# Kernel optimization log

Measured on AMD Instinct MI355X. Metric: run time of the kernel, lower is better.

Reference implementation:

```python
import jax, jax.numpy as jnp
import numpy as np


def pairwise_euclidean_distance(x, y):
    # x: [N, D], y: [K, D] -> [N, K] squared Euclidean distances
    cross = -2.0 * (x @ y.T)
    x_term = jnp.sum(x * x, axis=1, keepdims=True)      # [N, 1]
    y_term = jnp.sum(y * y, axis=1, keepdims=True).T    # [1, K]
    return cross + x_term + y_term


def quantize(z, centroids):
    # z: [B, T, D], centroids: [K, D]
    B, T, D = z.shape
    flat = z.reshape(-1, D)                              # [N, D]
    distances = pairwise_euclidean_distance(flat, centroids)
    alignment = jnp.argmin(distances, axis=1)            # [N]
    q = centroids[alignment]                             # gather [N, D]
    # straight-through estimator: grad flows to z, not centroids
    q = flat + jax.lax.stop_gradient(q - flat)
    return q.reshape(B, T, D)


def setup_inputs() -> dict:
    key = jax.random.key(0)
    ks = jax.random.split(key, 5)
    B, T, F, D, K = 16, 2048, 80, 512, 2048
    return {
        "x": jax.random.normal(ks[0], (B, T, F), dtype=jnp.float32),
        "W_enc": jax.random.normal(ks[1], (F, D), dtype=jnp.float32) * (1.0 / np.sqrt(F)),
        "b_enc": jnp.zeros((D,), dtype=jnp.float32),
        "centroids": jax.random.normal(ks[2], (K, D), dtype=jnp.float32),
        "W_dec": jax.random.normal(ks[3], (D, F), dtype=jnp.float32) * (1.0 / np.sqrt(D)),
        "b_dec": jnp.zeros((F,), dtype=jnp.float32),
    }


def reference(x, W_enc, b_enc, centroids, W_dec, b_dec):
    z = x @ W_enc + b_enc            # encoder: [B, T, D]
    zq = quantize(z, centroids)      # VQ: distance + argmin + gather
    out = zq @ W_dec + b_dec         # decoder: [B, T, F]
    return out
```

## Files before the change

kernel.cpp:

```cpp
#include <hip/hip_runtime.h>
#include <hip/hip_bf16.h>

#define N_TOK  32768
#define F_IN   80
#define D_DIM  512
#define K_CENT 2048
#define F_OUT  80
#define TM     16
#define KP     96
#define M2     0.5f
#define QSLOTS 24
#define QREC   200
#define TREC   800
#define JTOT   160

typedef __attribute__((ext_vector_type(8)))  short bf16x8;
typedef __attribute__((ext_vector_type(4)))  float fx4;
typedef __attribute__((ext_vector_type(16))) float fx16;

#define AS3 __attribute__((address_space(3)))
#define AS1 __attribute__((address_space(1)))

__device__ inline unsigned short f2bf(float f) {
    unsigned u = __float_as_uint(f);
    return (unsigned short)((u + 0x7FFFu + ((u >> 16) & 1u)) >> 16);
}
__device__ inline float bf2f(unsigned short h) {
    return __uint_as_float((unsigned)h << 16);
}

__device__ inline void gll16(const unsigned short* g, unsigned short* l) {
    __builtin_amdgcn_global_load_lds((const AS1 unsigned*)g, (AS3 unsigned*)l, 16, 0, 0);
}

__device__ inline unsigned fkey(float f) {
    unsigned b = __float_as_uint(f);
    return b ^ ((b >> 31) ? 0xFFFFFFFFu : 0x80000000u);
}
__device__ inline float keyf(unsigned k) {
    unsigned b = k ^ ((k & 0x80000000u) ? 0x80000000u : 0xFFFFFFFFu);
    return __uint_as_float(b);
}

__device__ inline size_t frag32_addr(int row, int k) {
    int sub = (row >> 5) * 2 + ((k >> 4) & 1);
    int L = (row & 31) + ((k >> 3) & 1) * 32;
    return (size_t)sub * 512 + L * 8 + (k & 7);
}

__global__ __launch_bounds__(256) void k_prep1(
    const float* __restrict__ x, const float* __restrict__ Wenc,
    const float* __restrict__ Wdec, const float* __restrict__ cent,
    const float* __restrict__ benc,
    unsigned short* __restrict__ xbt, float* __restrict__ Bcat,
    float* __restrict__ cnorm, unsigned short* __restrict__ Gbt) {
    const int bid = blockIdx.x, tid = threadIdx.x;
    if (bid < 1536) {
        int o = bid * 256 + tid;
        int m = o / 12;
        int ko = (o - m * 12) * 8;
        unsigned short u[8];
        if (ko < F_IN) {
            const float* src = x + (size_t)m * F_IN + ko;
            float4 v0 = *(const float4*)src;
            float4 v1 = *(const float4*)(src + 4);
            u[0]=f2bf(v0.x); u[1]=f2bf(v0.y); u[2]=f2bf(v0.z); u[3]=f2bf(v0.w);
            u[4]=f2bf(v1.x); u[5]=f2bf(v1.y); u[6]=f2bf(v1.z); u[7]=f2bf(v1.w);
        } else if (ko == 80) {
            u[0] = 0x3F80; u[1] = 0x3F80;
#pragma unroll
            for (int j = 2; j < 8; ++j) u[j] = 0;
        } else {
#pragma unroll
            for (int j = 0; j < 8; ++j) u[j] = 0;
        }
        int mt = m >> 7, kt = ko >> 5, row = m & 127, kl = ko & 31;
        uint4 p;
        p.x = (unsigned)u[0] | ((unsigned)u[1] << 16);
        p.y = (unsigned)u[2] | ((unsigned)u[3] << 16);
        p.z = (unsigned)u[4] | ((unsigned)u[5] << 16);
        p.w = (unsigned)u[6] | ((unsigned)u[7] << 16);
        *(uint4*)&xbt[(size_t)(mt * 3 + kt) * 4096 + frag32_addr(row, kl)] = p;
    } else if (bid < 1856) {
        int e = (bid - 1536) * 256 + tid;
        int d = e / JTOT, j = e - d * JTOT;
        float v = (j < F_OUT) ? Wdec[(size_t)d * F_OUT + j]
                              : Wenc[(size_t)(j - F_OUT) * D_DIM + d];
        Bcat[e] = v;
    } else {
        int wave = tid >> 6, lane = tid & 63;
        int k = (bid - 1856) * 4 + wave;
        const float* row = cent + (size_t)k * D_DIM;
        float s = 0.f, t = 0.f;
#pragma unroll
        for (int j = 0; j < 8; ++j) {
            float c = row[lane + 64 * j];
            float b = benc[lane + 64 * j];
            s += c * c; t += b * c;
        }
#pragma unroll
        for (int off = 32; off; off >>= 1) { s += __shfl_down(s, off); t += __shfl_down(t, off); }
        const int nt = k >> 7, cl = k & 127;
        const size_t tb = (size_t)(nt * 3 + 2) * 4096;
        if (lane < 14)
            Gbt[tb + frag32_addr(cl, 18 + lane)] = 0;
        if (lane == 0) {
            cnorm[k] = s;
            float v = -0.5f * (s - 2.0f * t);
            unsigned short h = f2bf(v);
            unsigned short l = f2bf(v - bf2f(h));
            Gbt[tb + frag32_addr(cl, 16)] = h;
            Gbt[tb + frag32_addr(cl, 17)] = l;
        }
    }
}

__global__ __launch_bounds__(384) void k_cgemm2(
    const float* __restrict__ cent, const float* __restrict__ Bcat,
    const float* __restrict__ bdec, unsigned short* __restrict__ Gbt,
    float* __restrict__ dec) {
    __shared__ float pacc[192][4];
    const int tid = threadIdx.x;
    const int j = tid % 192;
    const int dh = tid / 192;
    const int k0 = blockIdx.x * 4;
    float a0 = 0.f, a1 = 0.f, a2 = 0.f, a3 = 0.f;
    if (j < JTOT) {
        const float* c0 = cent + (size_t)k0 * D_DIM + dh * 256;
        const float* bp = Bcat + (size_t)dh * 256 * JTOT + j;
#pragma unroll 4
        for (int d = 0; d < 256; ++d) {
            float b  = bp[d * JTOT];
            a0 += c0[d] * b;
            a1 += c0[D_DIM + d] * b;
            a2 += c0[2 * D_DIM + d] * b;
            a3 += c0[3 * D_DIM + d] * b;
        }
        if (dh == 1) { pacc[j][0] = a0; pacc[j][1] = a1; pacc[j][2] = a2; pacc[j][3] = a3; }
    }
    __syncthreads();
    if (dh == 0 && j < JTOT) {
        a0 += pacc[j][0]; a1 += pacc[j][1]; a2 += pacc[j][2]; a3 += pacc[j][3];
        float a[4] = { a0, a1, a2, a3 };
        if (j < F_OUT) {
            float bd = bdec[j];
#pragma unroll
            for (int c = 0; c < 4; ++c)
                dec[(size_t)(k0 + c) * F_OUT + j] = a[c] + bd;
        } else {
            int f = j - F_OUT;
#pragma unroll
            for (int c = 0; c < 4; ++c) {
                int k = k0 + c;
                Gbt[(size_t)((k >> 7) * 3 + (f >> 5)) * 4096 + frag32_addr(k & 127, f & 31)]
                    = f2bf(a[c]);
            }
        }
    }
}

__global__ __launch_bounds__(512) void k_dist3(
    const unsigned short* __restrict__ xbt, const unsigned short* __restrict__ Gbt,
    char* __restrict__ lists) {
    __shared__ unsigned short Bs[2][12288];
    __shared__ int cnt[128];
    __shared__ unsigned mxk[128];

    const int tid = threadIdx.x;
    const int bid = blockIdx.x;
    const int mt = bid >> 2, nq = bid & 3;
    const int lane = tid & 63;
    const int wave = tid >> 6;
    const int tg = wave >> 1;
    const int ch = wave & 1;
    const int col = lane & 31;
    const int hi = lane >> 5;

    if (tid < 128) { cnt[tid] = 0; mxk[tid] = 0u; }

    bf16x8 bfr[6];
    const unsigned short* Ab = xbt + (size_t)mt * 12288;
#pragma unroll
    for (int kc = 0; kc < 6; ++kc)
        bfr[kc] = *(const bf16x8*)&Ab[(kc >> 1) * 4096 + (tg * 2 + (kc & 1)) * 512 + lane * 8];

    const int woff = (tid & ~63) * 8;
    const unsigned short* Gq = Gbt + (size_t)nq * 4 * 12288;
#pragma unroll
    for (int q = 0; q < 3; ++q)
        gll16(Gq + q * 4096 + tid * 8, &Bs[0][0] + q * 4096 + woff);

    float rmax = -3.4e38f;
    int cur = 0;
    for (int t4 = 0; t4 < 4; ++t4) {
        __syncthreads();
        if (t4 + 1 < 4) {
#pragma unroll
            for (int q = 0; q < 3; ++q)
                gll16(Gq + (size_t)(t4 + 1) * 12288 + q * 4096 + tid * 8,
                      &Bs[cur ^ 1][0] + q * 4096 + woff);
        }
        const unsigned short* B = &Bs[cur][0];
        fx16 acc[2];
#pragma unroll
        for (int u = 0; u < 2; ++u)
#pragma unroll
            for (int r = 0; r < 16; ++r) acc[u][r] = 0.f;
#pragma unroll
        for (int kc = 0; kc < 6; ++kc) {
#pragma unroll
            for (int u = 0; u < 2; ++u) {
                bf16x8 a = *(const bf16x8*)&B[(kc >> 1) * 4096
                             + ((ch * 2 + u) * 2 + (kc & 1)) * 512 + lane * 8];
                acc[u] = __builtin_amdgcn_mfma_f32_32x32x16_bf16(a, bfr[kc], acc[u], 0, 0, 0);
            }
        }
        float m = acc[0][0];
#pragma unroll
        for (int r = 1; r < 16; ++r) m = fmaxf(m, acc[0][r]);
#pragma unroll
        for (int r = 0; r < 16; ++r) m = fmaxf(m, acc[1][r]);
        m = fmaxf(m, __shfl_xor(m, 32));
        rmax = fmaxf(rmax, m);
        const float th = rmax - M2;
        const int tk = tg * 32 + col;
        char* qrec = lists + (size_t)(mt * 128 + tk) * TREC + nq * QREC;
#pragma unroll
        for (int u = 0; u < 2; ++u)
#pragma unroll
            for (int r = 0; r < 16; ++r) {
                float v = acc[u][r];
                if (v >= th) {
                    int slot = atomicAdd(&cnt[tk], 1);
                    if (slot < QSLOTS) {
                        uint2 e;
                        e.x = __float_as_uint(v);
                        e.y = (unsigned)((nq * 4 + t4) * 128 + (ch * 2 + u) * 32
                                         + (r & 3) + 8 * (r >> 2) + 4 * hi);
                        *(uint2*)(qrec + 8 + slot * 8) = e;
                    }
                }
            }
        cur ^= 1;
    }
    if (lane < 32) atomicMax(&mxk[tg * 32 + lane], fkey(rmax));
    __syncthreads();
    if (tid < 128) {
        uint2 h;
        h.x = (unsigned)cnt[tid];
        h.y = __float_as_uint(keyf(mxk[tid]));
        *(uint2*)(lists + (size_t)(mt * 128 + tid) * TREC + nq * QREC) = h;
    }
}

__global__ __launch_bounds__(256) void k_merge4(
    const char* __restrict__ lists, const float* __restrict__ cnorm,
    const float* __restrict__ cent, const float* __restrict__ x,
    const float* __restrict__ Wenc, const float* __restrict__ benc,
    const float* __restrict__ dec, float* __restrict__ out) {
    const int lane = threadIdx.x & 63;
    const int token = blockIdx.x * 4 + (threadIdx.x >> 6);
    const char* base = lists + (size_t)token * TREC;
    uint4 w4 = make_uint4(0u, 0u, 0u, 0u);
    if (lane < 50) w4 = *(const uint4*)(base + lane * 16);
    const int   c0 = __shfl((int)w4.x, 0),  c1 = __shfl((int)w4.z, 12);
    const int   c2 = __shfl((int)w4.x, 25), c3 = __shfl((int)w4.z, 37);
    const float m0 = __uint_as_float((unsigned)__shfl((int)w4.y, 0));
    const float m1 = __uint_as_float((unsigned)__shfl((int)w4.w, 12));
    const float m2 = __uint_as_float((unsigned)__shfl((int)w4.y, 25));
    const float m3 = __uint_as_float((unsigned)__shfl((int)w4.w, 37));
    const float gm = fmaxf(fmaxf(m0, m1), fmaxf(m2, m3));
    const float th = gm - M2;
    const bool ovf = (c0 > QSLOTS) || (c1 > QSLOTS) || (c2 > QSLOTS) || (c3 > QSLOTS);
    const int q0c = c0 < QSLOTS ? c0 : QSLOTS, q1c = c1 < QSLOTS ? c1 : QSLOTS;
    const int q2c = c2 < QSLOTS ? c2 : QSLOTS, q3c = c3 < QSLOTS ? c3 : QSLOTS;
    bool cd[2]; 
#pragma unroll
    for (int rr = 0; rr < 2; ++rr) {
        int t = lane * 2 + rr;
        int q = t / 25, s = t - q * 25;
        int cq = (q == 0) ? q0c : (q == 1) ? q1c : (q == 2) ? q2c : q3c;
        float v = __uint_as_float(rr ? w4.z : w4.x);
        cd[rr] = (lane < 50) && (s >= 1) && (s - 1 < cq) && (v >= th);
    }
    unsigned long long b0 = __ballot(cd[0]);
    unsigned long long b1 = __ballot(cd[1]);
    int ns = __popcll(b0) + __popcll(b1);
    int ans;
    if (!ovf && ns == 1) {
        if (b0) ans = __shfl((int)w4.y, __ffsll(b0) - 1);
        else    ans = __shfl((int)w4.w, __ffsll(b1) - 1);
    } else {
        float z8[8];
#pragma unroll
        for (int j = 0; j < 8; ++j) z8[j] = benc[lane * 8 + j];
        const float* xr = x + (size_t)token * F_IN;
        const float* wp = Wenc + lane * 8;
        for (int f = 0; f < F_IN; ++f) {
            float xf = xr[f];
            fx4 w0 = *(const fx4*)(wp + (size_t)f * D_DIM);
            fx4 w1 = *(const fx4*)(wp + (size_t)f * D_DIM + 4);
            z8[0] += xf * w0.x; z8[1] += xf * w0.y; z8[2] += xf * w0.z; z8[3] += xf * w0.w;
            z8[4] += xf * w1.x; z8[5] += xf * w1.y; z8[6] += xf * w1.z; z8[7] += xf * w1.w;
        }
        float bd = 1e30f; int bn = 0x7FFFFFFF;
        auto exact1 = [&](int ci) {
            const float* cr = cent + (size_t)ci * D_DIM + lane * 8;
            fx4 cc0 = *(const fx4*)cr, cc1 = *(const fx4*)(cr + 4);
            float dp = z8[0] * cc0.x + z8[1] * cc0.y + z8[2] * cc0.z + z8[3] * cc0.w
                     + z8[4] * cc1.x + z8[5] * cc1.y + z8[6] * cc1.z + z8[7] * cc1.w;
#pragma unroll
            for (int off = 1; off < 64; off <<= 1) dp += __shfl_xor(dp, off);
            float de = cnorm[ci] - 2.0f * dp;
            if (de < bd || (de == bd && ci < bn)) { bd = de; bn = ci; }
        };
        unsigned long long m = b0;
        while (m) { int src = __ffsll(m) - 1; m &= m - 1; exact1(__shfl((int)w4.y, src)); }
        m = b1;
        while (m) { int src = __ffsll(m) - 1; m &= m - 1; exact1(__shfl((int)w4.w, src)); }
        if (ovf) {
#pragma unroll
            for (int q = 0; q < 4; ++q) {
                int cf = (q == 0) ? c0 : (q == 1) ? c1 : (q == 2) ? c2 : c3;
                if (cf > QSLOTS)
                    for (int n0 = 0; n0 < 512; ++n0) exact1(q * 512 + n0);
            }
        }
        ans = bn;
    }
    const float* dr = dec + (size_t)ans * F_OUT;
    float* orow = out + (size_t)token * F_OUT;
    orow[lane] = dr[lane];
    if (lane < F_OUT - 64) orow[64 + lane] = dr[64 + lane];
}

__global__ void k_transpose(const float* __restrict__ cent, float* __restrict__ centT) {
    __shared__ float tile[64][65];
    int kb = blockIdx.x * 64, db = blockIdx.y * 64;
    int lx = threadIdx.x & 63, ly = threadIdx.x >> 6;
#pragma unroll
    for (int i = 0; i < 16; ++i) {
        int row = ly + i * 4;
        tile[row][lx] = cent[(size_t)(kb + row) * D_DIM + db + lx];
    }
    __syncthreads();
#pragma unroll
    for (int i = 0; i < 16; ++i) {
        int row = ly + i * 4;
        centT[(size_t)(db + row) * K_CENT + kb + lx] = tile[lx][row];
    }
}

__global__ void k_cnorm(const float* __restrict__ cent, float* __restrict__ cnorm) {
    int wave = threadIdx.x >> 6, lane = threadIdx.x & 63;
    int k = blockIdx.x * 4 + wave;
    const float* row = cent + (size_t)k * D_DIM;
    float s = 0.f;
#pragma unroll
    for (int j = 0; j < 8; ++j) { float v = row[lane + 64 * j]; s += v * v; }
#pragma unroll
    for (int off = 32; off; off >>= 1) s += __shfl_down(s, off);
    if (lane == 0) cnorm[k] = s;
}

__global__ void k_dec(const float* __restrict__ cent, const float* __restrict__ Wdec,
                      const float* __restrict__ bdec, float* __restrict__ dec) {
    __shared__ float cs[D_DIM];
    int k = blockIdx.x;
    for (int d = threadIdx.x; d < D_DIM; d += blockDim.x) cs[d] = cent[(size_t)k * D_DIM + d];
    __syncthreads();
    int f = threadIdx.x;
    if (f < F_OUT) {
        float a0 = 0.f, a1 = 0.f, a2 = 0.f, a3 = 0.f;
#pragma unroll 4
        for (int d = 0; d < D_DIM; d += 4) {
            a0 += cs[d + 0] * Wdec[(d + 0) * F_OUT + f];
            a1 += cs[d + 1] * Wdec[(d + 1) * F_OUT + f];
            a2 += cs[d + 2] * Wdec[(d + 2) * F_OUT + f];
            a3 += cs[d + 3] * Wdec[(d + 3) * F_OUT + f];
        }
        dec[(size_t)k * F_OUT + f] = a0 + a1 + a2 + a3 + bdec[f];
    }
}

__global__ void k_out(const float* __restrict__ dec, const int* __restrict__ idx,
                      float* __restrict__ out) {
    int e0 = blockIdx.x * 2560;
#pragma unroll
    for (int r = 0; r < 10; ++r) {
        int e = e0 + threadIdx.x + r * 256;
        int n = e / F_OUT, f = e - n * F_OUT;
        out[e] = dec[(size_t)idx[n] * F_OUT + f];
    }
}

__global__ __launch_bounds__(256) void k_main(
    const float* __restrict__ x, const float* __restrict__ Wenc,
    const float* __restrict__ benc, const float* __restrict__ centT,
    const float* __restrict__ cnorm, int* __restrict__ idxOut) {
    __shared__ float xs[TM * F_IN];
    __shared__ float zs[TM][D_DIM];
    float* pv = &zs[0][0];
    int*   pi = (int*)(&zs[0][0] + 256 * TM);
    const int tid = threadIdx.x;
    const int tok0 = blockIdx.x * TM;
    for (int e = tid; e < TM * F_IN; e += 256) xs[e] = x[(size_t)tok0 * F_IN + e];
    __syncthreads();
    {
        float acc0[TM], acc1[TM];
#pragma unroll
        for (int t = 0; t < TM; ++t) { acc0[t] = 0.f; acc1[t] = 0.f; }
        const float2 b2 = ((const float2*)benc)[tid];
#pragma unroll 4
        for (int f4 = 0; f4 < F_IN; f4 += 4) {
            float2 w0 = ((const float2*)(Wenc + (size_t)(f4 + 0) * D_DIM))[tid];
            float2 w1 = ((const float2*)(Wenc + (size_t)(f4 + 1) * D_DIM))[tid];
            float2 w2 = ((const float2*)(Wenc + (size_t)(f4 + 2) * D_DIM))[tid];
            float2 w3 = ((const float2*)(Wenc + (size_t)(f4 + 3) * D_DIM))[tid];
#pragma unroll
            for (int t = 0; t < TM; ++t) {
                float4 xv = *(const float4*)&xs[t * F_IN + f4];
                acc0[t] += xv.x * w0.x + xv.y * w1.x + xv.z * w2.x + xv.w * w3.x;
                acc1[t] += xv.x * w0.y + xv.y * w1.y + xv.z * w2.y + xv.w * w3.y;
            }
        }
#pragma unroll
        for (int t = 0; t < TM; ++t)
            *(float2*)&zs[t][2 * tid] = make_float2(acc0[t] + b2.x, acc1[t] + b2.y);
    }
    __syncthreads();
    float minv[TM]; int mini[TM];
#pragma unroll
    for (int t = 0; t < TM; ++t) { minv[t] = 3.4e38f; mini[t] = 0; }
    for (int iter = 0; iter < 2; ++iter) {
        float acc[4][TM];
#pragma unroll
        for (int j = 0; j < 4; ++j)
#pragma unroll
            for (int t = 0; t < TM; ++t) acc[j][t] = 0.f;
        const int cbase = iter * 1024 + tid;
        for (int d4 = 0; d4 < D_DIM; d4 += 4) {
            float cv[4][4];
#pragma unroll
            for (int dd = 0; dd < 4; ++dd) {
                const float* cp = centT + (size_t)(d4 + dd) * K_CENT + cbase;
                cv[dd][0] = cp[0]; cv[dd][1] = cp[256]; cv[dd][2] = cp[512]; cv[dd][3] = cp[768];
            }
#pragma unroll
            for (int t = 0; t < TM; ++t) {
                float4 zv = *(const float4*)&zs[t][d4];
#pragma unroll
                for (int j = 0; j < 4; ++j)
                    acc[j][t] += zv.x * cv[0][j] + zv.y * cv[1][j] + zv.z * cv[2][j] + zv.w * cv[3][j];
            }
        }
#pragma unroll
        for (int j = 0; j < 4; ++j) {
            int c = cbase + j * 256;
            float cn = cnorm[c];
#pragma unroll
            for (int t = 0; t < TM; ++t) {
                float dist = cn - 2.f * acc[j][t];
                if (dist < minv[t]) { minv[t] = dist; mini[t] = c; }
            }
        }
    }
    __syncthreads();
#pragma unroll
    for (int t = 0; t < TM; ++t) { pv[tid * TM + t] = minv[t]; pi[tid * TM + t] = mini[t]; }
    __syncthreads();
    {
        int t = tid & 15, g = tid >> 4;
        float bv = 3.4e38f; int bi = 0x7fffffff;
        for (int j = 0; j < 16; ++j) {
            int r2 = g + 16 * j;
            float vv = pv[r2 * TM + t]; int i2 = pi[r2 * TM + t];
            if (vv < bv || (vv == bv && i2 < bi)) { bv = vv; bi = i2; }
        }
        pv[g * TM + t] = bv; pi[g * TM + t] = bi;
    }
    __syncthreads();
    if (tid < TM) {
        int t = tid;
        float bv = 3.4e38f; int bi = 0x7fffffff;
        for (int g = 0; g < 16; ++g) {
            float vv = pv[g * TM + t]; int i2 = pi[g * TM + t];
            if (vv < bv || (vv == bv && i2 < bi)) { bv = vv; bi = i2; }
        }
        idxOut[tok0 + t] = bi;
    }
}

extern "C" void kernel_launch(void* const* d_in, const int* in_sizes, int n_in,
                              void* d_out, int out_size, void* d_ws, size_t ws_size,
                              hipStream_t stream) {
    const float* x    = (const float*)d_in[0];
    const float* Wenc = (const float*)d_in[1];
    const float* benc = (const float*)d_in[2];
    const float* cent = (const float*)d_in[3];
    const float* Wdec = (const float*)d_in[4];
    const float* bdec = (const float*)d_in[5];
    float* out = (float*)d_out;

    const size_t L_B  = (size_t)N_TOK * TREC;
    const size_t XB_B = (size_t)N_TOK * KP * 2;
    const size_t GB_B = (size_t)K_CENT * KP * 2;
    const size_t N_B  = (size_t)K_CENT * 4;
    const size_t D_B  = (size_t)K_CENT * F_OUT * 4;
    const size_t BC_B = (size_t)D_DIM * JTOT * 4;
    const size_t NEED = L_B + XB_B + GB_B + N_B + D_B + BC_B;

    if (ws_size >= NEED) {
        char* w = (char*)d_ws;
        char*           lists = w;                            w += L_B;
        unsigned short* xbt   = (unsigned short*)w;           w += XB_B;
        unsigned short* Gbt   = (unsigned short*)w;           w += GB_B;
        float*          cnorm = (float*)w;                    w += N_B;
        float*          dec   = (float*)w;                    w += D_B;
        float*          Bcat  = (float*)w;

        k_prep1<<<2368, 256, 0, stream>>>(x, Wenc, Wdec, cent, benc,
                                          xbt, Bcat, cnorm, Gbt);
        k_cgemm2<<<K_CENT / 4, 384, 0, stream>>>(cent, Bcat, bdec, Gbt, dec);
        k_dist3<<<1024, 512, 0, stream>>>(xbt, Gbt, lists);
        k_merge4<<<N_TOK / 4, 256, 0, stream>>>(lists, cnorm, cent, x, Wenc, benc, dec, out);
    } else {
        float* centT = (float*)d_ws;
        float* cnorm = centT + (size_t)D_DIM * K_CENT;
        float* dec   = cnorm + K_CENT;
        int*   idx   = (int*)(dec + (size_t)K_CENT * F_OUT);
        k_transpose<<<dim3(K_CENT / 64, D_DIM / 64), 256, 0, stream>>>(cent, centT);
        k_cnorm<<<K_CENT / 4, 256, 0, stream>>>(cent, cnorm);
        k_dec<<<K_CENT, 128, 0, stream>>>(cent, Wdec, bdec, dec);
        k_main<<<N_TOK / TM, 256, 0, stream>>>(x, Wenc, benc, centT, cnorm, idx);
        k_out<<<N_TOK * F_OUT / 2560, 256, 0, stream>>>(dec, idx, out);
    }
}
```

Baseline: 100.3 us.

## Convert x to bf16 inside distance kernel and apply centroid bias as fp32 epilogue

Drops the precomputed padded bf16 copy of x (xbt): the distance kernel now loads fp32 x directly and converts it to bf16 fragments in registers. The centroid-norm/bias term, previously packed as extra hi/lo bf16 K-columns appended through a ones-column in x, is instead subtracted in fp32 from the MFMA accumulators using a shared-memory table. This shrinks the reduction depth from 96 to 80 (6 to 5 MFMA steps), the G tile and LDS staging size, and removes a large prep pass and its global traffic. The trade-off is a per-element subtract in the epilogue plus strided fp32 loads of x in the distance kernel.

```diff
diff --git a/kernel.cpp b/kernel.cpp
--- a/kernel.cpp
+++ b/kernel.cpp
@@ -7,7 +7,6 @@
 #define K_CENT 2048
 #define F_OUT  80
 #define TM     16
-#define KP     96
 #define M2     0.5f
 #define QSLOTS 24
 #define QREC   200
@@ -25,9 +24,6 @@
     unsigned u = __float_as_uint(f);
     return (unsigned short)((u + 0x7FFFu + ((u >> 16) & 1u)) >> 16);
 }
-__device__ inline float bf2f(unsigned short h) {
-    return __uint_as_float((unsigned)h << 16);
-}
 
 __device__ inline void gll16(const unsigned short* g, unsigned short* l) {
     __builtin_amdgcn_global_load_lds((const AS1 unsigned*)g, (AS3 unsigned*)l, 16, 0, 0);
@@ -42,54 +38,24 @@
     return __uint_as_float(b);
 }
 
-__device__ inline size_t frag32_addr(int row, int k) {
-    int sub = (row >> 5) * 2 + ((k >> 4) & 1);
-    int L = (row & 31) + ((k >> 3) & 1) * 32;
-    return (size_t)sub * 512 + L * 8 + (k & 7);
-}
-
-__global__ __launch_bounds__(256) void k_prep1(
-    const float* __restrict__ x, const float* __restrict__ Wenc,
-    const float* __restrict__ Wdec, const float* __restrict__ cent,
-    const float* __restrict__ benc,
-    unsigned short* __restrict__ xbt, float* __restrict__ Bcat,
-    float* __restrict__ cnorm, unsigned short* __restrict__ Gbt) {
+__device__ inline size_t frag16_addr(int row, int k) {
+    return (size_t)(row >> 5) * 512 + (size_t)((row & 31) + ((k >> 3) << 5)) * 8 + (k & 7);
+}
+
+__global__ __launch_bounds__(256) void k_prep0(
+    const float* __restrict__ Wenc, const float* __restrict__ Wdec,
+    const float* __restrict__ cent, const float* __restrict__ benc,
+    float* __restrict__ Bcat, float* __restrict__ cnorm, float* __restrict__ cadjs) {
     const int bid = blockIdx.x, tid = threadIdx.x;
-    if (bid < 1536) {
-        int o = bid * 256 + tid;
-        int m = o / 12;
-        int ko = (o - m * 12) * 8;
-        unsigned short u[8];
-        if (ko < F_IN) {
-            const float* src = x + (size_t)m * F_IN + ko;
-            float4 v0 = *(const float4*)src;
-            float4 v1 = *(const float4*)(src + 4);
-            u[0]=f2bf(v0.x); u[1]=f2bf(v0.y); u[2]=f2bf(v0.z); u[3]=f2bf(v0.w);
-            u[4]=f2bf(v1.x); u[5]=f2bf(v1.y); u[6]=f2bf(v1.z); u[7]=f2bf(v1.w);
-        } else if (ko == 80) {
-            u[0] = 0x3F80; u[1] = 0x3F80;
-#pragma unroll
-            for (int j = 2; j < 8; ++j) u[j] = 0;
-        } else {
-#pragma unroll
-            for (int j = 0; j < 8; ++j) u[j] = 0;
-        }
-        int mt = m >> 7, kt = ko >> 5, row = m & 127, kl = ko & 31;
-        uint4 p;
-        p.x = (unsigned)u[0] | ((unsigned)u[1] << 16);
-        p.y = (unsigned)u[2] | ((unsigned)u[3] << 16);
-        p.z = (unsigned)u[4] | ((unsigned)u[5] << 16);
-        p.w = (unsigned)u[6] | ((unsigned)u[7] << 16);
-        *(uint4*)&xbt[(size_t)(mt * 3 + kt) * 4096 + frag32_addr(row, kl)] = p;
-    } else if (bid < 1856) {
-        int e = (bid - 1536) * 256 + tid;
+    if (bid < 320) {
+        int e = bid * 256 + tid;
         int d = e / JTOT, j = e - d * JTOT;
         float v = (j < F_OUT) ? Wdec[(size_t)d * F_OUT + j]
                               : Wenc[(size_t)(j - F_OUT) * D_DIM + d];
         Bcat[e] = v;
     } else {
         int wave = tid >> 6, lane = tid & 63;
-        int k = (bid - 1856) * 4 + wave;
+        int k = (bid - 320) * 4 + wave;
         const float* row = cent + (size_t)k * D_DIM;
         float s = 0.f, t = 0.f;
 #pragma unroll
@@ -100,17 +66,9 @@
         }
 #pragma unroll
         for (int off = 32; off; off >>= 1) { s += __shfl_down(s, off); t += __shfl_down(t, off); }
-        const int nt = k >> 7, cl = k & 127;
-        const size_t tb = (size_t)(nt * 3 + 2) * 4096;
-        if (lane < 14)
-            Gbt[tb + frag32_addr(cl, 18 + lane)] = 0;
         if (lane == 0) {
             cnorm[k] = s;
-            float v = -0.5f * (s - 2.0f * t);
-            unsigned short h = f2bf(v);
-            unsigned short l = f2bf(v - bf2f(h));
-            Gbt[tb + frag32_addr(cl, 16)] = h;
-            Gbt[tb + frag32_addr(cl, 17)] = l;
+            cadjs[k] = 0.5f * (s - 2.0f * t);
         }
     }
 }
@@ -152,17 +110,18 @@
 #pragma unroll
             for (int c = 0; c < 4; ++c) {
                 int k = k0 + c;
-                Gbt[(size_t)((k >> 7) * 3 + (f >> 5)) * 4096 + frag32_addr(k & 127, f & 31)]
-                    = f2bf(a[c]);
-            }
-        }
-    }
-}
-
-__global__ __launch_bounds__(512) void k_dist3(
-    const unsigned short* __restrict__ xbt, const unsigned short* __restrict__ Gbt,
-    char* __restrict__ lists) {
-    __shared__ unsigned short Bs[2][12288];
+                size_t tile = (size_t)((k >> 7) * 5 + (f >> 4));
+                Gbt[tile * 2048 + frag16_addr(k & 127, f & 15)] = f2bf(a[c]);
+            }
+        }
+    }
+}
+
+__global__ __launch_bounds__(512) void k_dist4(
+    const float* __restrict__ x, const unsigned short* __restrict__ Gbt,
+    const float* __restrict__ cadjs, char* __restrict__ lists) {
+    __shared__ unsigned short Bs[2][10240];
+    __shared__ float cadjq[512];
     __shared__ int cnt[128];
     __shared__ unsigned mxk[128];
 
@@ -177,28 +136,50 @@
     const int hi = lane >> 5;
 
     if (tid < 128) { cnt[tid] = 0; mxk[tid] = 0u; }
-
-    bf16x8 bfr[6];
-    const unsigned short* Ab = xbt + (size_t)mt * 12288;
-#pragma unroll
-    for (int kc = 0; kc < 6; ++kc)
-        bfr[kc] = *(const bf16x8*)&Ab[(kc >> 1) * 4096 + (tg * 2 + (kc & 1)) * 512 + lane * 8];
-
-    const int woff = (tid & ~63) * 8;
-    const unsigned short* Gq = Gbt + (size_t)nq * 4 * 12288;
-#pragma unroll
-    for (int q = 0; q < 3; ++q)
-        gll16(Gq + q * 4096 + tid * 8, &Bs[0][0] + q * 4096 + woff);
+    if (tid < 512) cadjq[tid] = cadjs[nq * 512 + tid];
+
+    bf16x8 bfr[5];
+    {
+        const int tok = mt * 128 + tg * 32 + col;
+        const float* xr = x + (size_t)tok * F_IN + hi * 8;
+#pragma unroll
+        for (int kc = 0; kc < 5; ++kc) {
+            float4 v0 = *(const float4*)(xr + kc * 16);
+            float4 v1 = *(const float4*)(xr + kc * 16 + 4);
+            bf16x8 t;
+            t[0] = (short)f2bf(v0.x); t[1] = (short)f2bf(v0.y);
+            t[2] = (short)f2bf(v0.z); t[3] = (short)f2bf(v0.w);
+            t[4] = (short)f2bf(v1.x); t[5] = (short)f2bf(v1.y);
+            t[6] = (short)f2bf(v1.z); t[7] = (short)f2bf(v1.w);
+            bfr[kc] = t;
+        }
+    }
+
+    const unsigned short* Gq = Gbt + (size_t)nq * 4 * 10240;
+    const unsigned short* dsl = 0;
+    {
+        const unsigned short* src = Gq;
+        unsigned short* dst = &Bs[0][0];
+#pragma unroll
+        for (int q = 0; q < 2; ++q)
+            gll16(src + q * 4096 + tid * 8, dst + q * 4096 + (tid & ~63) * 8);
+        if (tid < 256)
+            gll16(src + 8192 + tid * 8, dst + 8192 + (tid & ~63) * 8);
+    }
+    (void)dsl;
 
     float rmax = -3.4e38f;
     int cur = 0;
     for (int t4 = 0; t4 < 4; ++t4) {
         __syncthreads();
         if (t4 + 1 < 4) {
-#pragma unroll
-            for (int q = 0; q < 3; ++q)
-                gll16(Gq + (size_t)(t4 + 1) * 12288 + q * 4096 + tid * 8,
-                      &Bs[cur ^ 1][0] + q * 4096 + woff);
+            const unsigned short* src = Gq + (size_t)(t4 + 1) * 10240;
+            unsigned short* dst = &Bs[cur ^ 1][0];
+#pragma unroll
+            for (int q = 0; q < 2; ++q)
+                gll16(src + q * 4096 + tid * 8, dst + q * 4096 + (tid & ~63) * 8);
+            if (tid < 256)
+                gll16(src + 8192 + tid * 8, dst + 8192 + (tid & ~63) * 8);
         }
         const unsigned short* B = &Bs[cur][0];
         fx16 acc[2];
@@ -207,19 +188,26 @@
 #pragma unroll
             for (int r = 0; r < 16; ++r) acc[u][r] = 0.f;
 #pragma unroll
-        for (int kc = 0; kc < 6; ++kc) {
+        for (int kc = 0; kc < 5; ++kc) {
 #pragma unroll
             for (int u = 0; u < 2; ++u) {
-                bf16x8 a = *(const bf16x8*)&B[(kc >> 1) * 4096
-                             + ((ch * 2 + u) * 2 + (kc & 1)) * 512 + lane * 8];
+                bf16x8 a = *(const bf16x8*)&B[kc * 2048 + (ch * 2 + u) * 512 + lane * 8];
                 acc[u] = __builtin_amdgcn_mfma_f32_32x32x16_bf16(a, bfr[kc], acc[u], 0, 0, 0);
             }
         }
-        float m = acc[0][0];
-#pragma unroll
-        for (int r = 1; r < 16; ++r) m = fmaxf(m, acc[0][r]);
-#pragma unroll
-        for (int r = 0; r < 16; ++r) m = fmaxf(m, acc[1][r]);
+        float sc[2][16];
+#pragma unroll
+        for (int u = 0; u < 2; ++u)
+#pragma unroll
+            for (int r = 0; r < 16; ++r) {
+                int rowLoc = (ch * 2 + u) * 32 + (r & 3) + 8 * (r >> 2) + 4 * hi;
+                sc[u][r] = acc[u][r] - cadjq[t4 * 128 + rowLoc];
+            }
+        float m = sc[0][0];
+#pragma unroll
+        for (int r = 1; r < 16; ++r) m = fmaxf(m, sc[0][r]);
+#pragma unroll
+        for (int r = 0; r < 16; ++r) m = fmaxf(m, sc[1][r]);
         m = fmaxf(m, __shfl_xor(m, 32));
         rmax = fmaxf(rmax, m);
         const float th = rmax - M2;
@@ -229,13 +217,13 @@
         for (int u = 0; u < 2; ++u)
 #pragma unroll
             for (int r = 0; r < 16; ++r) {
-                float v = acc[u][r];
+                float v = sc[u][r];
                 if (v >= th) {
                     int slot = atomicAdd(&cnt[tk], 1);
                     if (slot < QSLOTS) {
                         uint2 e;
                         e.x = __float_as_uint(v);
-                        e.y = (unsigned)((nq * 4 + t4) * 128 + (ch * 2 + u) * 32
+                        e.y = (unsigned)(nq * 512 + t4 * 128 + (ch * 2 + u) * 32
                                          + (r & 3) + 8 * (r >> 2) + 4 * hi);
                         *(uint2*)(qrec + 8 + slot * 8) = e;
                     }
@@ -274,7 +262,7 @@
     const bool ovf = (c0 > QSLOTS) || (c1 > QSLOTS) || (c2 > QSLOTS) || (c3 > QSLOTS);
     const int q0c = c0 < QSLOTS ? c0 : QSLOTS, q1c = c1 < QSLOTS ? c1 : QSLOTS;
     const int q2c = c2 < QSLOTS ? c2 : QSLOTS, q3c = c3 < QSLOTS ? c3 : QSLOTS;
-    bool cd[2]; 
+    bool cd[2];
 #pragma unroll
     for (int rr = 0; rr < 2; ++rr) {
         int t = lane * 2 + rr;
@@ -503,26 +491,25 @@
     float* out = (float*)d_out;
 
     const size_t L_B  = (size_t)N_TOK * TREC;
-    const size_t XB_B = (size_t)N_TOK * KP * 2;
-    const size_t GB_B = (size_t)K_CENT * KP * 2;
+    const size_t GB_B = (size_t)K_CENT * F_IN * 2;
     const size_t N_B  = (size_t)K_CENT * 4;
+    const size_t A_B  = (size_t)K_CENT * 4;
     const size_t D_B  = (size_t)K_CENT * F_OUT * 4;
     const size_t BC_B = (size_t)D_DIM * JTOT * 4;
-    const size_t NEED = L_B + XB_B + GB_B + N_B + D_B + BC_B;
+    const size_t NEED = L_B + GB_B + N_B + A_B + D_B + BC_B;
 
     if (ws_size >= NEED) {
         char* w = (char*)d_ws;
         char*           lists = w;                            w += L_B;
-        unsigned short* xbt   = (unsigned short*)w;           w += XB_B;
         unsigned short* Gbt   = (unsigned short*)w;           w += GB_B;
         float*          cnorm = (float*)w;                    w += N_B;
+        float*          cadjs = (float*)w;                    w += A_B;
         float*          dec   = (float*)w;                    w += D_B;
         float*          Bcat  = (float*)w;
 
-        k_prep1<<<2368, 256, 0, stream>>>(x, Wenc, Wdec, cent, benc,
-                                          xbt, Bcat, cnorm, Gbt);
+        k_prep0<<<832, 256, 0, stream>>>(Wenc, Wdec, cent, benc, Bcat, cnorm, cadjs);
         k_cgemm2<<<K_CENT / 4, 384, 0, stream>>>(cent, Bcat, bdec, Gbt, dec);
-        k_dist3<<<1024, 512, 0, stream>>>(xbt, Gbt, lists);
+        k_dist4<<<1024, 512, 0, stream>>>(x, Gbt, cadjs, lists);
         k_merge4<<<N_TOK / 4, 256, 0, stream>>>(lists, cnorm, cent, x, Wenc, benc, dec, out);
     } else {
         float* centT = (float*)d_ws;
```

After: 118.4 us. 1.18x slower.
